# Kernel tuning notes

Measured on AMD Instinct MI355X. Metric: run time of the kernel, lower is better.

Reference implementation:

```python
import jax, jax.numpy as jnp
import numpy as np

SMOOTHING = 0.9  # NEURON_CONFIG['signal_smoothing']
NUM_SOURCE = 16384
NUM_TARGET = 16384
NUM_BRANCHES = 64
BATCH = 32


def setup_inputs() -> dict:
    key = jax.random.key(0)
    k1, k2, k3, k4 = jax.random.split(key, 4)
    spikes = jax.random.normal(k1, (BATCH, NUM_SOURCE), dtype=jnp.float32)
    attenuation = jax.random.uniform(k2, (NUM_SOURCE, NUM_BRANCHES), dtype=jnp.float32)
    target_indices = jax.random.randint(k3, (NUM_SOURCE, NUM_BRANCHES), 0, NUM_TARGET)
    delays = jax.random.randint(k4, (NUM_SOURCE, NUM_BRANCHES), 0, 6)
    return {"spikes": spikes, "attenuation": attenuation,
            "target_indices": target_indices, "delays": delays}


def reference(spikes, attenuation, target_indices, delays):
    # spikes: [B, S]; attenuation/delays/target_indices: [S, Br]
    B = spikes.shape[0]
    num_target = NUM_TARGET
    att = jnp.clip(attenuation, 0.0, 1.0)
    decay = SMOOTHING ** delays.astype(spikes.dtype)          # [S, Br]
    # fused elementwise: signal per (batch, source, branch)
    signals = spikes[:, :, None] * (att * decay)[None, :, :]   # [B, S, Br]
    flat_t = target_indices.reshape(-1)                        # [S*Br]
    flat_s = signals.reshape(B, -1)                            # [B, S*Br]
    out = jnp.zeros((B, num_target), dtype=spikes.dtype)
    out = out.at[jnp.arange(B)[:, None], flat_t[None, :]].add(flat_s)
    return out
```

## Files before the change

kernel.cpp:

```cpp
#include <hip/hip_runtime.h>

#define S_   16384
#define T_   16384
#define B_   32
#define NEDGES (S_ * 64)
#define GP_  256
#define EPG  4096
#define NBKT 512
#define TPB  32
#define CAPT 128
#define OVF_CAP 64

__device__ __forceinline__ float edge_weight(float a, int d) {
  float w = fminf(fmaxf(a, 0.0f), 1.0f);
  float r = (d & 1) ? 0.9f : 1.0f;
  r = (d & 2) ? r * 0.81f   : r;
  r = (d & 4) ? r * 0.6561f : r;
  return w * r;
}

__global__ __launch_bounds__(1024) void produce(
    const float* __restrict__ spikes,
    const float* __restrict__ att,
    const int*   __restrict__ tgt,
    const int*   __restrict__ del,
    float*        __restrict__ spikesT,
    int2*         __restrict__ rec,
    unsigned int* __restrict__ ofse) {
  __shared__ float tile[64][33];
  __shared__ int4  sbuf4[EPG / 2];
  __shared__ int   cnt5[NBKT], cur5[NBKT], sofs5[NBKT];
  __shared__ int   wtot[8];
  int2* buf = (int2*)sbuf4;

  const int g   = blockIdx.x;
  const int tid = threadIdx.x;
  if (tid < NBKT) cnt5[tid] = 0;

  const int s0 = g * 64;
  {
    const int x = tid & 63, y = tid >> 6;
    tile[x][y]      = spikes[(size_t)y        * S_ + s0 + x];
    tile[x][y + 16] = spikes[(size_t)(y + 16) * S_ + s0 + x];
  }

  const int e4  = g * 1024 + tid;
  int4   t = reinterpret_cast<const int4*>(tgt)[e4];
  float4 a = reinterpret_cast<const float4*>(att)[e4];
  int4   d = reinterpret_cast<const int4*>(del)[e4];
  const int src = (e4 * 4) >> 6;

  __syncthreads();

  {
    const int b = tid & 31, j = tid >> 5;
    spikesT[(size_t)(s0 + j)      * 32 + b] = tile[j][b];
    spikesT[(size_t)(s0 + j + 32) * 32 + b] = tile[j + 32][b];
  }

  const int bk0 = t.x >> 5, bk1 = t.y >> 5, bk2 = t.z >> 5, bk3 = t.w >> 5;
  __hip_atomic_fetch_add(&cnt5[bk0], 1, __ATOMIC_RELAXED, __HIP_MEMORY_SCOPE_WORKGROUP);
  __hip_atomic_fetch_add(&cnt5[bk1], 1, __ATOMIC_RELAXED, __HIP_MEMORY_SCOPE_WORKGROUP);
  __hip_atomic_fetch_add(&cnt5[bk2], 1, __ATOMIC_RELAXED, __HIP_MEMORY_SCOPE_WORKGROUP);
  __hip_atomic_fetch_add(&cnt5[bk3], 1, __ATOMIC_RELAXED, __HIP_MEMORY_SCOPE_WORKGROUP);
  __syncthreads();

  int v = 0, incl = 0;
  if (tid < NBKT) {
    v = cnt5[tid];
    incl = v;
#pragma unroll
    for (int off = 1; off < 64; off <<= 1) {
      int u = __shfl_up(incl, off);
      if ((tid & 63) >= off) incl += u;
    }
    if ((tid & 63) == 63) wtot[tid >> 6] = incl;
  }
  __syncthreads();
  if (tid < NBKT) {
    int base = 0;
    const int wv = tid >> 6;
    for (int i = 0; i < wv; ++i) base += wtot[i];
    const int start = base + incl - v;
    sofs5[tid] = start;
    cur5[tid]  = start;
  }
  __syncthreads();

#define PUT(BK, TL, AV, DV)                                                   \
  {                                                                           \
    int p = __hip_atomic_fetch_add(&cur5[BK], 1, __ATOMIC_RELAXED,            \
                                   __HIP_MEMORY_SCOPE_WORKGROUP);             \
    buf[p] = make_int2(((TL) << 14) | src,                                    \
                       __float_as_int(edge_weight((AV), (DV))));              \
  }
  PUT(bk0, t.x & 31, a.x, d.x)
  PUT(bk1, t.y & 31, a.y, d.y)
  PUT(bk2, t.z & 31, a.z, d.z)
  PUT(bk3, t.w & 31, a.w, d.w)
#undef PUT
  __syncthreads();

  int4* recO = reinterpret_cast<int4*>(rec) + (size_t)g * (EPG / 2);
  recO[tid]        = sbuf4[tid];
  recO[tid + 1024] = sbuf4[tid + 1024];
  if (tid < NBKT)
    ofse[(size_t)g * NBKT + tid] =
        ((unsigned)cur5[tid] << 16) | (unsigned)sofs5[tid];
}

__global__ __launch_bounds__(512) void consume(
    const int2*  __restrict__ rec,
    const unsigned int* __restrict__ ofse,
    const float* __restrict__ spikesT,
    float* __restrict__ out) {
  __shared__ int2  srt[TPB * CAPT];
  __shared__ float otile[TPB][33];
  __shared__ unsigned sse[GP_];
  __shared__ int   cur32[TPB];
  __shared__ int2  ovf[OVF_CAP];
  __shared__ int   ovfn;

  const int k   = blockIdx.x;
  const int tid = threadIdx.x;
  const int b   = tid & 31;
  const int hw  = tid >> 5;

  if (tid < TPB) cur32[tid] = tid * CAPT;
  if (tid == 0)  ovfn = 0;
  if (tid < GP_) sse[tid] = ofse[(size_t)tid * NBKT + k];
  __syncthreads();

  {
    const int grp = tid >> 3;
    const int l8  = tid & 7;
    for (int it = 0; it < 4; ++it) {
      const int g = grp + it * 64;
      const unsigned u = sse[g];
      const int st = (int)(u & 0xFFFF);
      const int n  = (int)(u >> 16) - st;
      const int2* slice = rec + (size_t)g * EPG + st;
      for (int j = l8; j < n; j += 8) {
        int2 r = slice[j];
        const int tl = (r.x >> 14) & 31;
        int p = __hip_atomic_fetch_add(&cur32[tl], 1, __ATOMIC_RELAXED,
                                       __HIP_MEMORY_SCOPE_WORKGROUP);
        if (p < (tl + 1) * CAPT) {
          srt[p] = r;
        } else {
          int q = __hip_atomic_fetch_add(&ovfn, 1, __ATOMIC_RELAXED,
                                         __HIP_MEMORY_SCOPE_WORKGROUP);
          if (q < OVF_CAP) ovf[q] = r;
        }
      }
    }
  }
  __syncthreads();

  float acc0 = 0.f, acc1 = 0.f;
  int e0 = hw * CAPT;
  int e1 = (hw + 16) * CAPT;
  const int e0e = min(cur32[hw],      (hw + 1)  * CAPT);
  const int e1e = min(cur32[hw + 16], (hw + 17) * CAPT);

  for (; e0 + 4 <= e0e && e1 + 4 <= e1e; e0 += 4, e1 += 4) {
    int2 r0 = srt[e0], r1 = srt[e0 + 1], r2 = srt[e0 + 2], r3 = srt[e0 + 3];
    int2 q0 = srt[e1], q1 = srt[e1 + 1], q2 = srt[e1 + 2], q3 = srt[e1 + 3];
    float s0 = spikesT[(size_t)(r0.x & 0x3FFF) * 32 + b];
    float s1 = spikesT[(size_t)(r1.x & 0x3FFF) * 32 + b];
    float s2 = spikesT[(size_t)(r2.x & 0x3FFF) * 32 + b];
    float s3 = spikesT[(size_t)(r3.x & 0x3FFF) * 32 + b];
    float u0 = spikesT[(size_t)(q0.x & 0x3FFF) * 32 + b];
    float u1 = spikesT[(size_t)(q1.x & 0x3FFF) * 32 + b];
    float u2 = spikesT[(size_t)(q2.x & 0x3FFF) * 32 + b];
    float u3 = spikesT[(size_t)(q3.x & 0x3FFF) * 32 + b];
    acc0 = fmaf(__int_as_float(r0.y), s0, acc0);
    acc0 = fmaf(__int_as_float(r1.y), s1, acc0);
    acc0 = fmaf(__int_as_float(r2.y), s2, acc0);
    acc0 = fmaf(__int_as_float(r3.y), s3, acc0);
    acc1 = fmaf(__int_as_float(q0.y), u0, acc1);
    acc1 = fmaf(__int_as_float(q1.y), u1, acc1);
    acc1 = fmaf(__int_as_float(q2.y), u2, acc1);
    acc1 = fmaf(__int_as_float(q3.y), u3, acc1);
  }
  for (; e0 + 4 <= e0e; e0 += 4) {
    int2 r0 = srt[e0], r1 = srt[e0 + 1], r2 = srt[e0 + 2], r3 = srt[e0 + 3];
    float s0 = spikesT[(size_t)(r0.x & 0x3FFF) * 32 + b];
    float s1 = spikesT[(size_t)(r1.x & 0x3FFF) * 32 + b];
    float s2 = spikesT[(size_t)(r2.x & 0x3FFF) * 32 + b];
    float s3 = spikesT[(size_t)(r3.x & 0x3FFF) * 32 + b];
    acc0 = fmaf(__int_as_float(r0.y), s0, acc0);
    acc0 = fmaf(__int_as_float(r1.y), s1, acc0);
    acc0 = fmaf(__int_as_float(r2.y), s2, acc0);
    acc0 = fmaf(__int_as_float(r3.y), s3, acc0);
  }
  for (; e0 < e0e; ++e0) {
    int2 r = srt[e0];
    acc0 = fmaf(__int_as_float(r.y), spikesT[(size_t)(r.x & 0x3FFF) * 32 + b], acc0);
  }
  for (; e1 + 4 <= e1e; e1 += 4) {
    int2 q0 = srt[e1], q1 = srt[e1 + 1], q2 = srt[e1 + 2], q3 = srt[e1 + 3];
    float u0 = spikesT[(size_t)(q0.x & 0x3FFF) * 32 + b];
    float u1 = spikesT[(size_t)(q1.x & 0x3FFF) * 32 + b];
    float u2 = spikesT[(size_t)(q2.x & 0x3FFF) * 32 + b];
    float u3 = spikesT[(size_t)(q3.x & 0x3FFF) * 32 + b];
    acc1 = fmaf(__int_as_float(q0.y), u0, acc1);
    acc1 = fmaf(__int_as_float(q1.y), u1, acc1);
    acc1 = fmaf(__int_as_float(q2.y), u2, acc1);
    acc1 = fmaf(__int_as_float(q3.y), u3, acc1);
  }
  for (; e1 < e1e; ++e1) {
    int2 q = srt[e1];
    acc1 = fmaf(__int_as_float(q.y), spikesT[(size_t)(q.x & 0x3FFF) * 32 + b], acc1);
  }

  const int no = min(ovfn, OVF_CAP);
  for (int j = 0; j < no; ++j) {
    int2 r = ovf[j];
    const int tl = (r.x >> 14) & 31;
    float s = spikesT[(size_t)(r.x & 0x3FFF) * 32 + b];
    float w = __int_as_float(r.y);
    if (tl == hw)      acc0 = fmaf(w, s, acc0);
    if (tl == hw + 16) acc1 = fmaf(w, s, acc1);
  }

  otile[hw][b]      = acc0;
  otile[hw + 16][b] = acc1;
  __syncthreads();
  const int bb = tid >> 4;
  const int cc = (tid & 15) * 2;
  float2 o2 = make_float2(otile[cc][bb], otile[cc + 1][bb]);
  *reinterpret_cast<float2*>(&out[(size_t)bb * T_ + k * 32 + cc]) = o2;
}

__global__ void zero_floats(float* __restrict__ p, int n) {
  int i = blockIdx.x * blockDim.x + threadIdx.x;
  if (i < n) p[i] = 0.0f;
}

__global__ void naive_kernel(const float* __restrict__ spikes,
                             const float* __restrict__ att,
                             const int*   __restrict__ tgt,
                             const int*   __restrict__ del,
                             float*       __restrict__ out) {
  int i = blockIdx.x * blockDim.x + threadIdx.x;
  if (i >= NEDGES) return;
  int   s = i >> 6;
  int   t = tgt[i];
  float w = edge_weight(att[i], del[i]);
  for (int b = 0; b < B_; ++b)
    unsafeAtomicAdd(&out[(size_t)b * T_ + t], w * spikes[(size_t)b * S_ + s]);
}

extern "C" void kernel_launch(void* const* d_in, const int* in_sizes, int n_in,
                              void* d_out, int out_size, void* d_ws, size_t ws_size,
                              hipStream_t stream) {
  const float* spikes = (const float*)d_in[0];
  const float* att    = (const float*)d_in[1];
  const int*   tgt    = (const int*)d_in[2];
  const int*   del    = (const int*)d_in[3];
  float*       out    = (float*)d_out;

  const size_t spikesT_bytes = (size_t)S_ * B_ * sizeof(float);
  const size_t rec_bytes     = (size_t)NEDGES * sizeof(int2);
  const size_t ofse_bytes    = (size_t)GP_ * NBKT * sizeof(unsigned);
  const size_t need = spikesT_bytes + rec_bytes + ofse_bytes + 64;

  if (ws_size < need) {
    zero_floats<<<(B_ * T_ + 255) / 256, 256, 0, stream>>>(out, B_ * T_);
    naive_kernel<<<(NEDGES + 255) / 256, 256, 0, stream>>>(spikes, att, tgt, del, out);
    return;
  }

  char* p = (char*)d_ws;
  float*        spikesT = (float*)p;        p += spikesT_bytes;
  int2*         rec     = (int2*)p;         p += rec_bytes;
  unsigned int* ofse    = (unsigned int*)p;

  produce<<<GP_, 1024, 0, stream>>>(spikes, att, tgt, del, spikesT, rec, ofse);
  consume<<<NBKT, 512, 0, stream>>>(rec, ofse, spikesT, out);
}
```

Measured before the change: 88.24 us.

## Fuse produce and consume into one cooperative kernel with grid sync

Merges the bucketing producer and the gather consumer into a single cooperative kernel that runs both phases, separated by a grid-wide barrier and a union of shared-memory layouts. This is meant to remove the second kernel launch and the gap between the two launches. To make the grid fit co-resident, producer groups shrink to 512 blocks of 512 threads, each handling 2048 edges. The consumer now reads 512 slices per bucket instead of 256. If cooperative launch is unavailable it falls back to two separate launches.

```diff
diff --git a/kernel.cpp b/kernel.cpp
--- a/kernel.cpp
+++ b/kernel.cpp
@@ -1,11 +1,14 @@
 #include <hip/hip_runtime.h>
+#include <hip/hip_cooperative_groups.h>
+
+namespace cg = cooperative_groups;
 
 #define S_   16384
 #define T_   16384
 #define B_   32
 #define NEDGES (S_ * 64)
-#define GP_  256
-#define EPG  4096
+#define GP_  512
+#define EPG  2048
 #define NBKT 512
 #define TPB  32
 #define CAPT 128
@@ -19,32 +22,39 @@
   return w * r;
 }
 
-__global__ __launch_bounds__(1024) void produce(
-    const float* __restrict__ spikes,
-    const float* __restrict__ att,
-    const int*   __restrict__ tgt,
-    const int*   __restrict__ del,
-    float*        __restrict__ spikesT,
-    int2*         __restrict__ rec,
+struct ProdSh {
+  float tile[32][33];
+  int2  buf[EPG];
+  int   cnt[NBKT], cur[NBKT], sofs[NBKT];
+  int   wtot[8];
+};
+struct ConsSh {
+  int2  srt[TPB * CAPT];
+  float otile[TPB][33];
+  unsigned sse[GP_];
+  int   cur32[TPB];
+  int2  ovf[OVF_CAP];
+  int   ovfn;
+};
+union SMem { ProdSh p; ConsSh c; };
+
+__device__ __forceinline__ void produce_phase(
+    SMem& smu, const int g, const int tid,
+    const float* __restrict__ spikes, const float* __restrict__ att,
+    const int* __restrict__ tgt, const int* __restrict__ del,
+    float* __restrict__ spikesT, int2* __restrict__ rec,
     unsigned int* __restrict__ ofse) {
-  __shared__ float tile[64][33];
-  __shared__ int4  sbuf4[EPG / 2];
-  __shared__ int   cnt5[NBKT], cur5[NBKT], sofs5[NBKT];
-  __shared__ int   wtot[8];
-  int2* buf = (int2*)sbuf4;
-
-  const int g   = blockIdx.x;
-  const int tid = threadIdx.x;
-  if (tid < NBKT) cnt5[tid] = 0;
-
-  const int s0 = g * 64;
+  ProdSh& sm = smu.p;
+  if (tid < NBKT) sm.cnt[tid] = 0;
+
+  const int s0 = g * 32;
   {
-    const int x = tid & 63, y = tid >> 6;
-    tile[x][y]      = spikes[(size_t)y        * S_ + s0 + x];
-    tile[x][y + 16] = spikes[(size_t)(y + 16) * S_ + s0 + x];
-  }
-
-  const int e4  = g * 1024 + tid;
+    const int x = tid & 31, y = tid >> 5;
+    sm.tile[x][y]      = spikes[(size_t)y        * S_ + s0 + x];
+    sm.tile[x][y + 16] = spikes[(size_t)(y + 16) * S_ + s0 + x];
+  }
+
+  const int e4  = g * 512 + tid;
   int4   t = reinterpret_cast<const int4*>(tgt)[e4];
   float4 a = reinterpret_cast<const float4*>(att)[e4];
   int4   d = reinterpret_cast<const int4*>(del)[e4];
@@ -54,45 +64,42 @@
 
   {
     const int b = tid & 31, j = tid >> 5;
-    spikesT[(size_t)(s0 + j)      * 32 + b] = tile[j][b];
-    spikesT[(size_t)(s0 + j + 32) * 32 + b] = tile[j + 32][b];
+    spikesT[(size_t)(s0 + j)      * 32 + b] = sm.tile[j][b];
+    spikesT[(size_t)(s0 + j + 16) * 32 + b] = sm.tile[j + 16][b];
   }
 
   const int bk0 = t.x >> 5, bk1 = t.y >> 5, bk2 = t.z >> 5, bk3 = t.w >> 5;
-  __hip_atomic_fetch_add(&cnt5[bk0], 1, __ATOMIC_RELAXED, __HIP_MEMORY_SCOPE_WORKGROUP);
-  __hip_atomic_fetch_add(&cnt5[bk1], 1, __ATOMIC_RELAXED, __HIP_MEMORY_SCOPE_WORKGROUP);
-  __hip_atomic_fetch_add(&cnt5[bk2], 1, __ATOMIC_RELAXED, __HIP_MEMORY_SCOPE_WORKGROUP);
-  __hip_atomic_fetch_add(&cnt5[bk3], 1, __ATOMIC_RELAXED, __HIP_MEMORY_SCOPE_WORKGROUP);
-  __syncthreads();
-
-  int v = 0, incl = 0;
-  if (tid < NBKT) {
-    v = cnt5[tid];
-    incl = v;
+  __hip_atomic_fetch_add(&sm.cnt[bk0], 1, __ATOMIC_RELAXED, __HIP_MEMORY_SCOPE_WORKGROUP);
+  __hip_atomic_fetch_add(&sm.cnt[bk1], 1, __ATOMIC_RELAXED, __HIP_MEMORY_SCOPE_WORKGROUP);
+  __hip_atomic_fetch_add(&sm.cnt[bk2], 1, __ATOMIC_RELAXED, __HIP_MEMORY_SCOPE_WORKGROUP);
+  __hip_atomic_fetch_add(&sm.cnt[bk3], 1, __ATOMIC_RELAXED, __HIP_MEMORY_SCOPE_WORKGROUP);
+  __syncthreads();
+
+  int v = sm.cnt[tid];
+  int incl = v;
 #pragma unroll
-    for (int off = 1; off < 64; off <<= 1) {
-      int u = __shfl_up(incl, off);
-      if ((tid & 63) >= off) incl += u;
-    }
-    if ((tid & 63) == 63) wtot[tid >> 6] = incl;
-  }
-  __syncthreads();
-  if (tid < NBKT) {
+  for (int off = 1; off < 64; off <<= 1) {
+    int u = __shfl_up(incl, off);
+    if ((tid & 63) >= off) incl += u;
+  }
+  if ((tid & 63) == 63) sm.wtot[tid >> 6] = incl;
+  __syncthreads();
+  {
     int base = 0;
     const int wv = tid >> 6;
-    for (int i = 0; i < wv; ++i) base += wtot[i];
+    for (int i = 0; i < wv; ++i) base += sm.wtot[i];
     const int start = base + incl - v;
-    sofs5[tid] = start;
-    cur5[tid]  = start;
+    sm.sofs[tid] = start;
+    sm.cur[tid]  = start;
   }
   __syncthreads();
 
 #define PUT(BK, TL, AV, DV)                                                   \
   {                                                                           \
-    int p = __hip_atomic_fetch_add(&cur5[BK], 1, __ATOMIC_RELAXED,            \
+    int p = __hip_atomic_fetch_add(&sm.cur[BK], 1, __ATOMIC_RELAXED,          \
                                    __HIP_MEMORY_SCOPE_WORKGROUP);             \
-    buf[p] = make_int2(((TL) << 14) | src,                                    \
-                       __float_as_int(edge_weight((AV), (DV))));              \
+    sm.buf[p] = make_int2(((TL) << 14) | src,                                 \
+                          __float_as_int(edge_weight((AV), (DV))));           \
   }
   PUT(bk0, t.x & 31, a.x, d.x)
   PUT(bk1, t.y & 31, a.y, d.y)
@@ -101,56 +108,47 @@
 #undef PUT
   __syncthreads();
 
+  const int4* sbuf4 = reinterpret_cast<const int4*>(sm.buf);
   int4* recO = reinterpret_cast<int4*>(rec) + (size_t)g * (EPG / 2);
-  recO[tid]        = sbuf4[tid];
-  recO[tid + 1024] = sbuf4[tid + 1024];
-  if (tid < NBKT)
-    ofse[(size_t)g * NBKT + tid] =
-        ((unsigned)cur5[tid] << 16) | (unsigned)sofs5[tid];
-}
-
-__global__ __launch_bounds__(512) void consume(
-    const int2*  __restrict__ rec,
-    const unsigned int* __restrict__ ofse,
-    const float* __restrict__ spikesT,
-    float* __restrict__ out) {
-  __shared__ int2  srt[TPB * CAPT];
-  __shared__ float otile[TPB][33];
-  __shared__ unsigned sse[GP_];
-  __shared__ int   cur32[TPB];
-  __shared__ int2  ovf[OVF_CAP];
-  __shared__ int   ovfn;
-
-  const int k   = blockIdx.x;
-  const int tid = threadIdx.x;
-  const int b   = tid & 31;
-  const int hw  = tid >> 5;
-
-  if (tid < TPB) cur32[tid] = tid * CAPT;
-  if (tid == 0)  ovfn = 0;
-  if (tid < GP_) sse[tid] = ofse[(size_t)tid * NBKT + k];
+  recO[tid]       = sbuf4[tid];
+  recO[tid + 512] = sbuf4[tid + 512];
+  ofse[(size_t)g * NBKT + tid] =
+      ((unsigned)sm.cur[tid] << 16) | (unsigned)sm.sofs[tid];
+}
+
+__device__ __forceinline__ void consume_phase(
+    SMem& smu, const int k, const int tid,
+    const int2* __restrict__ rec, const unsigned int* __restrict__ ofse,
+    const float* __restrict__ spikesT, float* __restrict__ out) {
+  ConsSh& sm = smu.c;
+  const int b  = tid & 31;
+  const int hw = tid >> 5;
+
+  if (tid < TPB) sm.cur32[tid] = tid * CAPT;
+  if (tid == 0)  sm.ovfn = 0;
+  sm.sse[tid] = ofse[(size_t)tid * NBKT + k];
   __syncthreads();
 
   {
-    const int grp = tid >> 3;
-    const int l8  = tid & 7;
+    const int grp = tid >> 2;
+    const int l4  = tid & 3;
     for (int it = 0; it < 4; ++it) {
-      const int g = grp + it * 64;
-      const unsigned u = sse[g];
+      const int g = grp + it * 128;
+      const unsigned u = sm.sse[g];
       const int st = (int)(u & 0xFFFF);
       const int n  = (int)(u >> 16) - st;
       const int2* slice = rec + (size_t)g * EPG + st;
-      for (int j = l8; j < n; j += 8) {
+      for (int j = l4; j < n; j += 4) {
         int2 r = slice[j];
         const int tl = (r.x >> 14) & 31;
-        int p = __hip_atomic_fetch_add(&cur32[tl], 1, __ATOMIC_RELAXED,
+        int p = __hip_atomic_fetch_add(&sm.cur32[tl], 1, __ATOMIC_RELAXED,
                                        __HIP_MEMORY_SCOPE_WORKGROUP);
         if (p < (tl + 1) * CAPT) {
-          srt[p] = r;
+          sm.srt[p] = r;
         } else {
-          int q = __hip_atomic_fetch_add(&ovfn, 1, __ATOMIC_RELAXED,
+          int q = __hip_atomic_fetch_add(&sm.ovfn, 1, __ATOMIC_RELAXED,
                                          __HIP_MEMORY_SCOPE_WORKGROUP);
-          if (q < OVF_CAP) ovf[q] = r;
+          if (q < OVF_CAP) sm.ovf[q] = r;
         }
       }
     }
@@ -160,12 +158,12 @@
   float acc0 = 0.f, acc1 = 0.f;
   int e0 = hw * CAPT;
   int e1 = (hw + 16) * CAPT;
-  const int e0e = min(cur32[hw],      (hw + 1)  * CAPT);
-  const int e1e = min(cur32[hw + 16], (hw + 17) * CAPT);
+  const int e0e = min(sm.cur32[hw],      (hw + 1)  * CAPT);
+  const int e1e = min(sm.cur32[hw + 16], (hw + 17) * CAPT);
 
   for (; e0 + 4 <= e0e && e1 + 4 <= e1e; e0 += 4, e1 += 4) {
-    int2 r0 = srt[e0], r1 = srt[e0 + 1], r2 = srt[e0 + 2], r3 = srt[e0 + 3];
-    int2 q0 = srt[e1], q1 = srt[e1 + 1], q2 = srt[e1 + 2], q3 = srt[e1 + 3];
+    int2 r0 = sm.srt[e0], r1 = sm.srt[e0 + 1], r2 = sm.srt[e0 + 2], r3 = sm.srt[e0 + 3];
+    int2 q0 = sm.srt[e1], q1 = sm.srt[e1 + 1], q2 = sm.srt[e1 + 2], q3 = sm.srt[e1 + 3];
     float s0 = spikesT[(size_t)(r0.x & 0x3FFF) * 32 + b];
     float s1 = spikesT[(size_t)(r1.x & 0x3FFF) * 32 + b];
     float s2 = spikesT[(size_t)(r2.x & 0x3FFF) * 32 + b];
@@ -184,7 +182,7 @@
     acc1 = fmaf(__int_as_float(q3.y), u3, acc1);
   }
   for (; e0 + 4 <= e0e; e0 += 4) {
-    int2 r0 = srt[e0], r1 = srt[e0 + 1], r2 = srt[e0 + 2], r3 = srt[e0 + 3];
+    int2 r0 = sm.srt[e0], r1 = sm.srt[e0 + 1], r2 = sm.srt[e0 + 2], r3 = sm.srt[e0 + 3];
     float s0 = spikesT[(size_t)(r0.x & 0x3FFF) * 32 + b];
     float s1 = spikesT[(size_t)(r1.x & 0x3FFF) * 32 + b];
     float s2 = spikesT[(size_t)(r2.x & 0x3FFF) * 32 + b];
@@ -195,11 +193,11 @@
     acc0 = fmaf(__int_as_float(r3.y), s3, acc0);
   }
   for (; e0 < e0e; ++e0) {
-    int2 r = srt[e0];
+    int2 r = sm.srt[e0];
     acc0 = fmaf(__int_as_float(r.y), spikesT[(size_t)(r.x & 0x3FFF) * 32 + b], acc0);
   }
   for (; e1 + 4 <= e1e; e1 += 4) {
-    int2 q0 = srt[e1], q1 = srt[e1 + 1], q2 = srt[e1 + 2], q3 = srt[e1 + 3];
+    int2 q0 = sm.srt[e1], q1 = sm.srt[e1 + 1], q2 = sm.srt[e1 + 2], q3 = sm.srt[e1 + 3];
     float u0 = spikesT[(size_t)(q0.x & 0x3FFF) * 32 + b];
     float u1 = spikesT[(size_t)(q1.x & 0x3FFF) * 32 + b];
     float u2 = spikesT[(size_t)(q2.x & 0x3FFF) * 32 + b];
@@ -210,13 +208,13 @@
     acc1 = fmaf(__int_as_float(q3.y), u3, acc1);
   }
   for (; e1 < e1e; ++e1) {
-    int2 q = srt[e1];
+    int2 q = sm.srt[e1];
     acc1 = fmaf(__int_as_float(q.y), spikesT[(size_t)(q.x & 0x3FFF) * 32 + b], acc1);
   }
 
-  const int no = min(ovfn, OVF_CAP);
+  const int no = min(sm.ovfn, OVF_CAP);
   for (int j = 0; j < no; ++j) {
-    int2 r = ovf[j];
+    int2 r = sm.ovf[j];
     const int tl = (r.x >> 14) & 31;
     float s = spikesT[(size_t)(r.x & 0x3FFF) * 32 + b];
     float w = __int_as_float(r.y);
@@ -224,13 +222,42 @@
     if (tl == hw + 16) acc1 = fmaf(w, s, acc1);
   }
 
-  otile[hw][b]      = acc0;
-  otile[hw + 16][b] = acc1;
+  sm.otile[hw][b]      = acc0;
+  sm.otile[hw + 16][b] = acc1;
   __syncthreads();
   const int bb = tid >> 4;
   const int cc = (tid & 15) * 2;
-  float2 o2 = make_float2(otile[cc][bb], otile[cc + 1][bb]);
+  float2 o2 = make_float2(sm.otile[cc][bb], sm.otile[cc + 1][bb]);
   *reinterpret_cast<float2*>(&out[(size_t)bb * T_ + k * 32 + cc]) = o2;
+}
+
+__global__ __launch_bounds__(512, 4) void fused(
+    const float* __restrict__ spikes, const float* __restrict__ att,
+    const int* __restrict__ tgt, const int* __restrict__ del,
+    float* __restrict__ spikesT, int2* __restrict__ rec,
+    unsigned int* __restrict__ ofse, float* __restrict__ out) {
+  __shared__ SMem sm;
+  produce_phase(sm, blockIdx.x, threadIdx.x, spikes, att, tgt, del,
+                spikesT, rec, ofse);
+  __threadfence();
+  cg::this_grid().sync();
+  consume_phase(sm, blockIdx.x, threadIdx.x, rec, ofse, spikesT, out);
+}
+
+__global__ __launch_bounds__(512) void produce_k(
+    const float* __restrict__ spikes, const float* __restrict__ att,
+    const int* __restrict__ tgt, const int* __restrict__ del,
+    float* __restrict__ spikesT, int2* __restrict__ rec,
+    unsigned int* __restrict__ ofse) {
+  __shared__ SMem sm;
+  produce_phase(sm, blockIdx.x, threadIdx.x, spikes, att, tgt, del,
+                spikesT, rec, ofse);
+}
+__global__ __launch_bounds__(512) void consume_k(
+    const int2* __restrict__ rec, const unsigned int* __restrict__ ofse,
+    const float* __restrict__ spikesT, float* __restrict__ out) {
+  __shared__ SMem sm;
+  consume_phase(sm, blockIdx.x, threadIdx.x, rec, ofse, spikesT, out);
 }
 
 __global__ void zero_floats(float* __restrict__ p, int n) {
@@ -277,6 +304,26 @@
   int2*         rec     = (int2*)p;         p += rec_bytes;
   unsigned int* ofse    = (unsigned int*)p;
 
-  produce<<<GP_, 1024, 0, stream>>>(spikes, att, tgt, del, spikesT, rec, ofse);
-  consume<<<NBKT, 512, 0, stream>>>(rec, ofse, spikesT, out);
-}
+  static int coop_ok = -1;
+  if (coop_ok < 0) {
+    int dev = 0;
+    hipGetDevice(&dev);
+    hipDeviceProp_t prop;
+    hipGetDeviceProperties(&prop, dev);
+    int nb = 0;
+    hipOccupancyMaxActiveBlocksPerMultiprocessor(&nb, fused, 512, 0);
+    coop_ok = (prop.cooperativeLaunch && nb * prop.multiProcessorCount >= GP_) ? 1 : 0;
+  }
+
+  if (coop_ok) {
+    void* args[] = {(void*)&spikes, (void*)&att, (void*)&tgt, (void*)&del,
+                    (void*)&spikesT, (void*)&rec, (void*)&ofse, (void*)&out};
+    hipError_t rc = hipLaunchCooperativeKernel((const void*)fused, dim3(GP_),
+                                               dim3(512), args, 0, stream);
+    if (rc == hipSuccess) return;
+    coop_ok = 0;
+  }
+
+  produce_k<<<GP_, 512, 0, stream>>>(spikes, att, tgt, del, spikesT, rec, ofse);
+  consume_k<<<NBKT, 512, 0, stream>>>(rec, ofse, spikesT, out);
+}
```

Measured after the change: 220.7 us. +150.1%, slower.
